# Kernel optimization log

Measured on AMD Instinct MI355X. Metric: run time of the kernel, lower is better.

Reference implementation:

```python
import jax, jax.numpy as jnp
import numpy as np

N_USERS = 50000
N_ITEMS = 50000
N = N_USERS + N_ITEMS
DIM = 64
N_LAYERS = 3
N_EDGES = 1250000
BN_EPS = 1e-5


def setup_inputs() -> dict:
    key = jax.random.key(0)
    k_x, k_e, k_w, k_b = jax.random.split(key, 4)
    x = jax.random.normal(k_x, (N, DIM), dtype=jnp.float32)
    edge_index = jax.random.randint(k_e, (2, N_EDGES), 0, N, dtype=jnp.int64)
    # Glorot-ish init for the per-layer GCNConv linear weights [L, DIM, DIM]
    Ws = jax.random.normal(k_w, (N_LAYERS, DIM, DIM), dtype=jnp.float32) * (1.0 / np.sqrt(DIM))
    bs = jnp.zeros((N_LAYERS, DIM), dtype=jnp.float32)
    gamma = jnp.ones((DIM,), dtype=jnp.float32)
    beta = jnp.zeros((DIM,), dtype=jnp.float32)
    return {"x": x, "edge_index": edge_index, "Ws": Ws, "bs": bs,
            "gamma": gamma, "beta": beta}


def _gcn_conv(x, W, b, src, dst, deg_inv_sqrt):
    # PyG GCNConv: h = x @ W^T ; out_i = sum_{j->i} norm_ji * h_j + b
    h = x @ W.T                                   # [N, DIM]
    norm = deg_inv_sqrt[src] * deg_inv_sqrt[dst]  # [E2]
    msg = h[src] * norm[:, None]                  # gather over irregular edges
    out = jax.ops.segment_sum(msg, dst, num_segments=N)
    return out + b


def reference(x, edge_index, Ws, bs, gamma, beta):
    # Add self-loops once (same augmented graph for every layer).
    loops = jnp.arange(N, dtype=edge_index.dtype)
    src = jnp.concatenate([edge_index[0], loops])  # source nodes j
    dst = jnp.concatenate([edge_index[1], loops])  # target nodes i
    # Symmetric normalization degrees (edge weight 1, counted at targets).
    deg = jax.ops.segment_sum(jnp.ones_like(dst, dtype=x.dtype), dst, num_segments=N)
    deg_inv_sqrt = jnp.where(deg > 0, jax.lax.rsqrt(deg), 0.0)

    for i in range(N_LAYERS):
        x = _gcn_conv(x, Ws[i], bs[i], src, dst, deg_inv_sqrt)

    # BatchNorm1d (training-mode batch statistics, biased variance)
    mean = jnp.mean(x, axis=0)
    var = jnp.mean((x - mean) ** 2, axis=0)
    x = (x - mean) * jax.lax.rsqrt(var + BN_EPS) * gamma + beta

    users, items = x[:N_USERS], x[N_USERS:]
    return users, items
```

## Files before the change

### kernel.cpp

```cpp
#include <hip/hip_runtime.h>

#define NN      100000
#define NUSERS  50000
#define NE      1250000
#define DIM     64
#define BN_EPS  1e-5f
#define NBUCK   8
#define NCHUNK  256
#define SLOT    40
#define CPAD    8

typedef __attribute__((ext_vector_type(8))) short s16x8;
typedef __attribute__((ext_vector_type(4))) float f32x4;

__device__ __forceinline__ short f2b(float f) {
    unsigned u = __builtin_bit_cast(unsigned, f);
    u = (u + 0x7fffu + ((u >> 16) & 1u)) >> 16;
    return (short)u;
}
__device__ __forceinline__ float b2f(unsigned short s) {
    unsigned u = ((unsigned)s) << 16;
    return __builtin_bit_cast(float, u);
}

__global__ __launch_bounds__(256) void place_part(const int* __restrict__ ei,
                                                  int* __restrict__ cursor,
                                                  int* __restrict__ csr_src) {
    int lane = threadIdx.x & 63, wave = threadIdx.x >> 6;
    int B = blockIdx.x & (NBUCK - 1);
    int gw = (blockIdx.x >> 3) * 4 + wave;
    const int NW = NCHUNK * 4;
    int gwr = gw + B * (NW / NBUCK);
    if (gwr >= NW) gwr -= NW;
    const int per = (NE + NW - 1) / NW;
    int e0 = gwr * per;
    int e1 = e0 + per; if (e1 > NE) e1 = NE;
    for (int eb = e0; eb < e1; eb += 8 * 64) {
        int d[8], s[8];
        bool k[8];
#pragma unroll
        for (int u = 0; u < 8; ++u) {
            int ee = eb + u * 64 + lane;
            bool in = ee < e1;
            int idx = in ? ee : e0;
            d[u] = ei[NE + idx];
            s[u] = ei[idx];
            k[u] = in && ((d[u] / 12500) == B);
        }
#pragma unroll
        for (int u = 0; u < 8; ++u) {
            if (k[u]) {
                int pos = atomicAdd(&cursor[d[u] * CPAD], 1);
                if (pos < SLOT) csr_src[d[u] * SLOT + pos] = s[u];
            }
        }
    }
}

__global__ __launch_bounds__(256) void dinv_c0(const int* __restrict__ cursor,
                                               float* __restrict__ dinv,
                                               const float* __restrict__ Ws,
                                               const float* __restrict__ bs,
                                               float* __restrict__ c0) {
    int v = blockIdx.x * blockDim.x + threadIdx.x;
    if (v < NN) dinv[v] = rsqrtf((float)cursor[v * CPAD] + 1.0f);
    if (v < 128) {
        int l = v >> 6, j = v & 63;
        const float* Wl = Ws + (size_t)(l + 1) * 4096;
        const float* bl = bs + l * 64;
        float s = 0.0f;
        for (int k = 0; k < 64; ++k) s += bl[k] * Wl[j * 64 + k];
        c0[v] = s;
    }
}

template <int L0>
__global__ __launch_bounds__(256) void gemm_mfma(const void* __restrict__ Xin,
                                                 const float* __restrict__ W,
                                                 const float* __restrict__ dinv,
                                                 const float* __restrict__ c0,
                                                 unsigned short* __restrict__ Gb) {
    __shared__ s16x8 WL[8][64];
    int lane = threadIdx.x & 63;
    int n16 = lane & 15, quad = lane >> 4;

#pragma unroll
    for (int e = threadIdx.x; e < 512; e += 256) {
        int ln = e & 63, tc = e >> 6;
        int tt = tc >> 1, cc = tc & 1;
        int m16 = ln & 15, qq = ln >> 4;
        const float4* wp = (const float4*)(W + (tt * 16 + m16) * 64 + cc * 32 + qq * 8);
        float4 w0 = wp[0], w1 = wp[1];
        s16x8 f;
        f[0] = f2b(w0.x); f[1] = f2b(w0.y); f[2] = f2b(w0.z); f[3] = f2b(w0.w);
        f[4] = f2b(w1.x); f[5] = f2b(w1.y); f[6] = f2b(w1.z); f[7] = f2b(w1.w);
        WL[tc][ln] = f;
    }
    __syncthreads();

    s16x8 bfrag[4][2];
#pragma unroll
    for (int t = 0; t < 4; ++t)
#pragma unroll
        for (int c = 0; c < 2; ++c)
            bfrag[t][c] = WL[t * 2 + c][lane];

    int wid = (blockIdx.x * blockDim.x + threadIdx.x) >> 6;
    int nw  = (gridDim.x * blockDim.x) >> 6;
    for (int tile = wid; tile < NN / 16; tile += nw) {
        int r0 = tile * 16;
        int m  = r0 + n16;
        s16x8 a[2];
#pragma unroll
        for (int c = 0; c < 2; ++c) {
            if (L0) {
                const float4* xp = (const float4*)((const float*)Xin + (size_t)m * 64 + c * 32 + quad * 8);
                float4 x0 = xp[0], x1 = xp[1];
                s16x8 f;
                f[0] = f2b(x0.x); f[1] = f2b(x0.y); f[2] = f2b(x0.z); f[3] = f2b(x0.w);
                f[4] = f2b(x1.x); f[5] = f2b(x1.y); f[6] = f2b(x1.z); f[7] = f2b(x1.w);
                a[c] = f;
            } else {
                a[c] = *(const s16x8*)((const unsigned short*)Xin + (size_t)m * 64 + c * 32 + quad * 8);
            }
        }
        f32x4 acc[4] = {{0,0,0,0},{0,0,0,0},{0,0,0,0},{0,0,0,0}};
#pragma unroll
        for (int c = 0; c < 2; ++c)
#pragma unroll
            for (int t = 0; t < 4; ++t)
                acc[t] = __builtin_amdgcn_mfma_f32_16x16x32_bf16(a[c], bfrag[t][c], acc[t], 0, 0, 0);

        float dvr[4];
#pragma unroll
        for (int r = 0; r < 4; ++r) dvr[r] = dinv[r0 + quad * 4 + r];
#pragma unroll
        for (int t = 0; t < 4; ++t) {
            float cc = L0 ? 0.0f : c0[t * 16 + n16];
#pragma unroll
            for (int r = 0; r < 4; ++r) {
                float dv = dvr[r];
                float g  = L0 ? dv * acc[t][r] : dv * dv * acc[t][r] + dv * cc;
                Gb[(size_t)(r0 + quad * 4 + r) * 64 + t * 16 + n16] = (unsigned short)f2b(g);
            }
        }
    }
}

template <int BASE>
__device__ __forceinline__ void gbatch8(const unsigned short* __restrict__ Gb,
                                        int v, int c, int g, int n, int ir,
                                        float& ax, float& ay, float& az, float& aw) {
    ushort4 val[8];
    float msk[8];
#pragma unroll
    for (int u = 0; u < 8; ++u) {
        int j = BASE + u;
        int s = __shfl(ir, g * 16 + (j & 15), 64);
        bool ok = j < n;
        msk[u] = ok ? 1.0f : 0.0f;
        val[u] = *(const ushort4*)(Gb + (size_t)(ok ? s : v) * 64 + c * 4);
    }
#pragma unroll
    for (int u = 0; u < 8; ++u) {
        ax = fmaf(msk[u], b2f(val[u].x), ax);
        ay = fmaf(msk[u], b2f(val[u].y), ay);
        az = fmaf(msk[u], b2f(val[u].z), az);
        aw = fmaf(msk[u], b2f(val[u].w), aw);
    }
}

__global__ __launch_bounds__(256) void gather_q(const int* __restrict__ cursor,
                                                const int* __restrict__ csr_src,
                                                const unsigned short* __restrict__ Gb,
                                                unsigned short* __restrict__ ACCb) {
    int lane = threadIdx.x & 63;
    int c = lane & 15, g = lane >> 4;
    int wid  = (blockIdx.x * blockDim.x + threadIdx.x) >> 6;
    int v4 = wid * 4;
    if (v4 >= NN) return;
    int v = v4 + g;
    int n = cursor[v * CPAD]; if (n > SLOT) n = SLOT;
    int i0 = csr_src[v * SLOT + c];
    ushort4 sv = *(const ushort4*)(Gb + (size_t)v * 64 + c * 4);
    float ax = b2f(sv.x), ay = b2f(sv.y), az = b2f(sv.z), aw = b2f(sv.w);
    if (n > 0)  gbatch8<0 >(Gb, v, c, g, n, i0, ax, ay, az, aw);
    if (n > 8)  gbatch8<8 >(Gb, v, c, g, n, i0, ax, ay, az, aw);
    if (n > 16) {
        int i1 = csr_src[v * SLOT + 16 + c];
        gbatch8<16>(Gb, v, c, g, n, i1, ax, ay, az, aw);
        if (n > 24) gbatch8<24>(Gb, v, c, g, n, i1, ax, ay, az, aw);
        if (n > 32) {
            int i2 = csr_src[v * SLOT + 32 + (c & 7)];
            gbatch8<32>(Gb, v, c, g, n, i2, ax, ay, az, aw);
        }
    }
    ushort4 o;
    o.x = (unsigned short)f2b(ax); o.y = (unsigned short)f2b(ay);
    o.z = (unsigned short)f2b(az); o.w = (unsigned short)f2b(aw);
    *(ushort4*)(ACCb + (size_t)v * 64 + c * 4) = o;
}

__global__ __launch_bounds__(256) void bn_stats(const unsigned short* __restrict__ ACCb,
                                                const float* __restrict__ dinv,
                                                const float* __restrict__ blast,
                                                float* __restrict__ sums) {
    int j = threadIdx.x & 63;
    float b = blast[j];
    int wid = (blockIdx.x * blockDim.x + threadIdx.x) >> 6;
    int nw  = (gridDim.x * blockDim.x) >> 6;
    float s = 0.0f, s2 = 0.0f;
    for (int v = wid; v < NN; v += nw) {
        float y = dinv[v] * b2f(ACCb[(size_t)v * 64 + j]) + b;
        s += y;
        s2 += y * y;
    }
    __shared__ float ls[256], ls2[256];
    ls[threadIdx.x] = s;
    ls2[threadIdx.x] = s2;
    __syncthreads();
    if (threadIdx.x < 64) {
        s  = ls[threadIdx.x] + ls[threadIdx.x + 64] + ls[threadIdx.x + 128] + ls[threadIdx.x + 192];
        s2 = ls2[threadIdx.x] + ls2[threadIdx.x + 64] + ls2[threadIdx.x + 128] + ls2[threadIdx.x + 192];
        atomicAdd(&sums[j], s);
        atomicAdd(&sums[64 + j], s2);
    }
}

__global__ __launch_bounds__(256) void bn_apply(const unsigned short* __restrict__ ACCb,
                                                const float* __restrict__ dinv,
                                                const float* __restrict__ blast,
                                                const float* __restrict__ sums,
                                                const float* __restrict__ gamma,
                                                const float* __restrict__ beta,
                                                float* __restrict__ out) {
    const float invN = 1.0f / (float)NN;
    int stride = gridDim.x * blockDim.x;
    for (int i = blockIdx.x * blockDim.x + threadIdx.x; i < NN * 64; i += stride) {
        int j = i & 63;
        int v = i >> 6;
        float mean = sums[j] * invN;
        float var  = sums[64 + j] * invN - mean * mean;
        float y = dinv[v] * b2f(ACCb[i]) + blast[j];
        out[i] = (y - mean) * rsqrtf(var + BN_EPS) * gamma[j] + beta[j];
    }
}

extern "C" void kernel_launch(void* const* d_in, const int* in_sizes, int n_in,
                              void* d_out, int out_size, void* d_ws, size_t ws_size,
                              hipStream_t stream) {
    const float* x     = (const float*)d_in[0];
    const int*   ei    = (const int*)d_in[1];
    const float* Ws    = (const float*)d_in[2];
    const float* bs    = (const float*)d_in[3];
    const float* gamma = (const float*)d_in[4];
    const float* beta  = (const float*)d_in[5];
    float* out = (float*)d_out;

    char* ws = (char*)d_ws;
    size_t off = 0;
    unsigned short* ACCb = (unsigned short*)(ws + off); off += (size_t)NN * 64 * 2;
    unsigned short* Gb   = (unsigned short*)(ws + off); off += (size_t)NN * 64 * 2;
    float* dinv    = (float*)(ws + off); off += (size_t)NN * 4;
    float* sums    = (float*)(ws + off); off += 128 * 4;
    float* c0      = (float*)(ws + off); off += 128 * 4;
    int*   cursor  = (int*)(ws + off);   off += (size_t)NN * CPAD * 4;
    int*   csr_src = (int*)(ws + off);   off += (size_t)NN * SLOT * 4;

    hipMemsetAsync(cursor, 0, (size_t)NN * CPAD * sizeof(int), stream);
    hipMemsetAsync(sums, 0, 128 * sizeof(float), stream);

    place_part<<<NBUCK * NCHUNK, 256, 0, stream>>>(ei, cursor, csr_src);
    dinv_c0<<<(NN + 255) / 256, 256, 0, stream>>>(cursor, dinv, Ws, bs, c0);

    gemm_mfma<1><<<1563, 256, 0, stream>>>(x, Ws, dinv, nullptr, Gb);
    gather_q<<<6250, 256, 0, stream>>>(cursor, csr_src, Gb, ACCb);
    for (int l = 1; l < 3; ++l) {
        gemm_mfma<0><<<1563, 256, 0, stream>>>(ACCb, Ws + (size_t)l * 4096, dinv,
                                               c0 + (l - 1) * 64, Gb);
        gather_q<<<6250, 256, 0, stream>>>(cursor, csr_src, Gb, ACCb);
    }

    bn_stats<<<2048, 256, 0, stream>>>(ACCb, dinv, bs + 128, sums);
    bn_apply<<<2048, 256, 0, stream>>>(ACCb, dinv, bs + 128, sums, gamma, beta, out);
}
```

Baseline: 329.6 us.

## Fuse next-layer GEMM into gather kernel epilogue with ping-pong buffers

Each gather block now aggregates 16 nodes, stages the fp32 sums in shared memory, and has one wave run the next layer's 64x64 MFMA transform before writing the pre-scaled bf16 features. This removes the two standalone GEMM launches and the bf16 round trip of the aggregated features through global memory. It uses ping-pong feature buffers so a fused gather never overwrites the array it reads. In exchange every gather block reloads and converts W into LDS, adds a block barrier, and leaves three of four waves idle during the epilogue.

```diff
diff --git a/kernel.cpp b/kernel.cpp
--- a/kernel.cpp
+++ b/kernel.cpp
@@ -74,12 +74,10 @@
     }
 }
 
-template <int L0>
-__global__ __launch_bounds__(256) void gemm_mfma(const void* __restrict__ Xin,
-                                                 const float* __restrict__ W,
-                                                 const float* __restrict__ dinv,
-                                                 const float* __restrict__ c0,
-                                                 unsigned short* __restrict__ Gb) {
+__global__ __launch_bounds__(256) void gemm_l0(const float* __restrict__ Xin,
+                                               const float* __restrict__ W,
+                                               const float* __restrict__ dinv,
+                                               unsigned short* __restrict__ Gb) {
     __shared__ s16x8 WL[8][64];
     int lane = threadIdx.x & 63;
     int n16 = lane & 15, quad = lane >> 4;
@@ -113,16 +111,12 @@
         s16x8 a[2];
 #pragma unroll
         for (int c = 0; c < 2; ++c) {
-            if (L0) {
-                const float4* xp = (const float4*)((const float*)Xin + (size_t)m * 64 + c * 32 + quad * 8);
-                float4 x0 = xp[0], x1 = xp[1];
-                s16x8 f;
-                f[0] = f2b(x0.x); f[1] = f2b(x0.y); f[2] = f2b(x0.z); f[3] = f2b(x0.w);
-                f[4] = f2b(x1.x); f[5] = f2b(x1.y); f[6] = f2b(x1.z); f[7] = f2b(x1.w);
-                a[c] = f;
-            } else {
-                a[c] = *(const s16x8*)((const unsigned short*)Xin + (size_t)m * 64 + c * 32 + quad * 8);
-            }
+            const float4* xp = (const float4*)(Xin + (size_t)m * 64 + c * 32 + quad * 8);
+            float4 x0 = xp[0], x1 = xp[1];
+            s16x8 f;
+            f[0] = f2b(x0.x); f[1] = f2b(x0.y); f[2] = f2b(x0.z); f[3] = f2b(x0.w);
+            f[4] = f2b(x1.x); f[5] = f2b(x1.y); f[6] = f2b(x1.z); f[7] = f2b(x1.w);
+            a[c] = f;
         }
         f32x4 acc[4] = {{0,0,0,0},{0,0,0,0},{0,0,0,0},{0,0,0,0}};
 #pragma unroll
@@ -135,15 +129,11 @@
 #pragma unroll
         for (int r = 0; r < 4; ++r) dvr[r] = dinv[r0 + quad * 4 + r];
 #pragma unroll
-        for (int t = 0; t < 4; ++t) {
-            float cc = L0 ? 0.0f : c0[t * 16 + n16];
-#pragma unroll
-            for (int r = 0; r < 4; ++r) {
-                float dv = dvr[r];
-                float g  = L0 ? dv * acc[t][r] : dv * dv * acc[t][r] + dv * cc;
-                Gb[(size_t)(r0 + quad * 4 + r) * 64 + t * 16 + n16] = (unsigned short)f2b(g);
-            }
-        }
+        for (int t = 0; t < 4; ++t)
+#pragma unroll
+            for (int r = 0; r < 4; ++r)
+                Gb[(size_t)(r0 + quad * 4 + r) * 64 + t * 16 + n16] =
+                    (unsigned short)f2b(dvr[r] * acc[t][r]);
     }
 }
 
@@ -170,35 +160,102 @@
     }
 }
 
-__global__ __launch_bounds__(256) void gather_q(const int* __restrict__ cursor,
-                                                const int* __restrict__ csr_src,
-                                                const unsigned short* __restrict__ Gb,
-                                                unsigned short* __restrict__ ACCb) {
-    int lane = threadIdx.x & 63;
+template <int FUSE>
+__global__ __launch_bounds__(256) void gather_fused(const int* __restrict__ cursor,
+                                                    const int* __restrict__ csr_src,
+                                                    const unsigned short* __restrict__ Gb_in,
+                                                    const float* __restrict__ W,
+                                                    const float* __restrict__ dinv,
+                                                    const float* __restrict__ c0,
+                                                    unsigned short* __restrict__ outp) {
+    __shared__ s16x8 WL[8][64];
+    __shared__ float AT[16][68];
+    int lane = threadIdx.x & 63, wave = threadIdx.x >> 6;
     int c = lane & 15, g = lane >> 4;
-    int wid  = (blockIdx.x * blockDim.x + threadIdx.x) >> 6;
-    int v4 = wid * 4;
-    if (v4 >= NN) return;
-    int v = v4 + g;
+
+    if (FUSE) {
+#pragma unroll
+        for (int e = threadIdx.x; e < 512; e += 256) {
+            int ln = e & 63, tc = e >> 6;
+            int tt = tc >> 1, cc2 = tc & 1;
+            int m16 = ln & 15, qq = ln >> 4;
+            const float4* wp = (const float4*)(W + (tt * 16 + m16) * 64 + cc2 * 32 + qq * 8);
+            float4 w0 = wp[0], w1 = wp[1];
+            s16x8 f;
+            f[0] = f2b(w0.x); f[1] = f2b(w0.y); f[2] = f2b(w0.z); f[3] = f2b(w0.w);
+            f[4] = f2b(w1.x); f[5] = f2b(w1.y); f[6] = f2b(w1.z); f[7] = f2b(w1.w);
+            WL[tc][ln] = f;
+        }
+    }
+
+    int r0 = blockIdx.x * 16;
+    int v  = r0 + wave * 4 + g;
     int n = cursor[v * CPAD]; if (n > SLOT) n = SLOT;
     int i0 = csr_src[v * SLOT + c];
-    ushort4 sv = *(const ushort4*)(Gb + (size_t)v * 64 + c * 4);
+    ushort4 sv = *(const ushort4*)(Gb_in + (size_t)v * 64 + c * 4);
     float ax = b2f(sv.x), ay = b2f(sv.y), az = b2f(sv.z), aw = b2f(sv.w);
-    if (n > 0)  gbatch8<0 >(Gb, v, c, g, n, i0, ax, ay, az, aw);
-    if (n > 8)  gbatch8<8 >(Gb, v, c, g, n, i0, ax, ay, az, aw);
+    if (n > 0)  gbatch8<0 >(Gb_in, v, c, g, n, i0, ax, ay, az, aw);
+    if (n > 8)  gbatch8<8 >(Gb_in, v, c, g, n, i0, ax, ay, az, aw);
     if (n > 16) {
         int i1 = csr_src[v * SLOT + 16 + c];
-        gbatch8<16>(Gb, v, c, g, n, i1, ax, ay, az, aw);
-        if (n > 24) gbatch8<24>(Gb, v, c, g, n, i1, ax, ay, az, aw);
+        gbatch8<16>(Gb_in, v, c, g, n, i1, ax, ay, az, aw);
+        if (n > 24) gbatch8<24>(Gb_in, v, c, g, n, i1, ax, ay, az, aw);
         if (n > 32) {
             int i2 = csr_src[v * SLOT + 32 + (c & 7)];
-            gbatch8<32>(Gb, v, c, g, n, i2, ax, ay, az, aw);
-        }
-    }
-    ushort4 o;
-    o.x = (unsigned short)f2b(ax); o.y = (unsigned short)f2b(ay);
-    o.z = (unsigned short)f2b(az); o.w = (unsigned short)f2b(aw);
-    *(ushort4*)(ACCb + (size_t)v * 64 + c * 4) = o;
+            gbatch8<32>(Gb_in, v, c, g, n, i2, ax, ay, az, aw);
+        }
+    }
+
+    if (!FUSE) {
+        ushort4 o;
+        o.x = (unsigned short)f2b(ax); o.y = (unsigned short)f2b(ay);
+        o.z = (unsigned short)f2b(az); o.w = (unsigned short)f2b(aw);
+        *(ushort4*)(outp + (size_t)v * 64 + c * 4) = o;
+        return;
+    }
+
+    float4 f4; f4.x = ax; f4.y = ay; f4.z = az; f4.w = aw;
+    *(float4*)&AT[wave * 4 + g][c * 4] = f4;
+    __syncthreads();
+    if (wave != 0) return;
+
+    int n16 = lane & 15, quad = lane >> 4;
+    s16x8 a[2];
+#pragma unroll
+    for (int cc2 = 0; cc2 < 2; ++cc2) {
+        const float* ap = &AT[n16][cc2 * 32 + quad * 8];
+        s16x8 f;
+#pragma unroll
+        for (int q2 = 0; q2 < 8; ++q2) f[q2] = f2b(ap[q2]);
+        a[cc2] = f;
+    }
+    s16x8 bfrag[4][2];
+#pragma unroll
+    for (int t = 0; t < 4; ++t)
+#pragma unroll
+        for (int cc2 = 0; cc2 < 2; ++cc2)
+            bfrag[t][cc2] = WL[t * 2 + cc2][lane];
+
+    f32x4 acc[4] = {{0,0,0,0},{0,0,0,0},{0,0,0,0},{0,0,0,0}};
+#pragma unroll
+    for (int cc2 = 0; cc2 < 2; ++cc2)
+#pragma unroll
+        for (int t = 0; t < 4; ++t)
+            acc[t] = __builtin_amdgcn_mfma_f32_16x16x32_bf16(a[cc2], bfrag[t][cc2], acc[t], 0, 0, 0);
+
+    float dvr[4];
+#pragma unroll
+    for (int r = 0; r < 4; ++r) dvr[r] = dinv[r0 + quad * 4 + r];
+#pragma unroll
+    for (int t = 0; t < 4; ++t) {
+        float cc2 = c0[t * 16 + n16];
+#pragma unroll
+        for (int r = 0; r < 4; ++r) {
+            float dv = dvr[r];
+            float g2 = dv * dv * acc[t][r] + dv * cc2;
+            outp[(size_t)(r0 + quad * 4 + r) * 64 + t * 16 + n16] = (unsigned short)f2b(g2);
+        }
+    }
 }
 
 __global__ __launch_bounds__(256) void bn_stats(const unsigned short* __restrict__ ACCb,
@@ -260,7 +317,8 @@
     char* ws = (char*)d_ws;
     size_t off = 0;
     unsigned short* ACCb = (unsigned short*)(ws + off); off += (size_t)NN * 64 * 2;
-    unsigned short* Gb   = (unsigned short*)(ws + off); off += (size_t)NN * 64 * 2;
+    unsigned short* GbA  = (unsigned short*)(ws + off); off += (size_t)NN * 64 * 2;
+    unsigned short* GbB  = (unsigned short*)(ws + off); off += (size_t)NN * 64 * 2;
     float* dinv    = (float*)(ws + off); off += (size_t)NN * 4;
     float* sums    = (float*)(ws + off); off += 128 * 4;
     float* c0      = (float*)(ws + off); off += 128 * 4;
@@ -273,13 +331,13 @@
     place_part<<<NBUCK * NCHUNK, 256, 0, stream>>>(ei, cursor, csr_src);
     dinv_c0<<<(NN + 255) / 256, 256, 0, stream>>>(cursor, dinv, Ws, bs, c0);
 
-    gemm_mfma<1><<<1563, 256, 0, stream>>>(x, Ws, dinv, nullptr, Gb);
-    gather_q<<<6250, 256, 0, stream>>>(cursor, csr_src, Gb, ACCb);
-    for (int l = 1; l < 3; ++l) {
-        gemm_mfma<0><<<1563, 256, 0, stream>>>(ACCb, Ws + (size_t)l * 4096, dinv,
-                                               c0 + (l - 1) * 64, Gb);
-        gather_q<<<6250, 256, 0, stream>>>(cursor, csr_src, Gb, ACCb);
-    }
+    gemm_l0<<<1563, 256, 0, stream>>>(x, Ws, dinv, GbA);
+    gather_fused<1><<<6250, 256, 0, stream>>>(cursor, csr_src, GbA,
+                                              Ws + 4096, dinv, c0, GbB);
+    gather_fused<1><<<6250, 256, 0, stream>>>(cursor, csr_src, GbB,
+                                              Ws + 8192, dinv, c0 + 64, GbA);
+    gather_fused<0><<<6250, 256, 0, stream>>>(cursor, csr_src, GbA,
+                                              nullptr, nullptr, nullptr, ACCb);
 
     bn_stats<<<2048, 256, 0, stream>>>(ACCb, dinv, bs + 128, sums);
     bn_apply<<<2048, 256, 0, stream>>>(ACCb, dinv, bs + 128, sums, gamma, beta, out);
```

Measured after the change: 316.1 us, median of 2. 4.1% less time.
